# Kernel optimization log

Measured on AMD Instinct MI355X. Metric: run time of the kernel, lower is better.

## Reference

```python
import jax, jax.numpy as jnp
import numpy as np

IMG_H, IMG_W = 800.0, 1280.0
STRIDE = 16
SCALE = 1.0 / STRIDE
P, S = 14, 1              # pooler resolution, sampling ratio
NUM_CLASSES = 80
BBOX_W = (10.0, 10.0, 5.0, 5.0)
SCORE_TH, NMS_TH, MAX_DET, IOU_TH = 0.05, 0.5, 100, 0.5
SCALE_CLAMP = float(np.log(1000.0 / 16.0))


def _make_boxes(key, n_img, n_box):
    k1, k2, k3, k4 = jax.random.split(key, 4)
    x1 = jax.random.uniform(k1, (n_img, n_box)) * (IMG_W - 64.0)
    y1 = jax.random.uniform(k2, (n_img, n_box)) * (IMG_H - 64.0)
    w = jax.random.uniform(k3, (n_img, n_box)) * 300.0 + 16.0
    h = jax.random.uniform(k4, (n_img, n_box)) * 300.0 + 16.0
    x2 = jnp.minimum(x1 + w, IMG_W)
    y2 = jnp.minimum(y1 + h, IMG_H)
    return jnp.stack([x1, y1, x2, y2], axis=-1)


def setup_inputs() -> dict:
    key = jax.random.key(0)
    ks = jax.random.split(key, 6)
    features = jax.random.normal(ks[0], (2, 50, 80, 1024), dtype=jnp.float32)
    proposals = _make_boxes(ks[1], 2, 256)
    gt_boxes = _make_boxes(ks[2], 2, 64)
    gt_classes = jax.random.randint(ks[3], (2, 64), 0, NUM_CLASSES)
    W_cls = jax.random.normal(ks[4], (1024, NUM_CLASSES + 1), dtype=jnp.float32) * 0.01
    b_cls = jnp.zeros((NUM_CLASSES + 1,), jnp.float32)
    W_box = jax.random.normal(ks[5], (1024, 4), dtype=jnp.float32) * 0.01
    b_box = jnp.zeros((4,), jnp.float32)
    return {"features": features, "proposals": proposals, "gt_boxes": gt_boxes,
            "gt_classes": gt_classes, "W_cls": W_cls, "b_cls": b_cls,
            "W_box": W_box, "b_box": b_box}


def pairwise_iou(a, b):
    # a: [G,4], b: [R,4], boxes as (x1,y1,x2,y2) -> [G,R]
    area_a = (a[:, 2] - a[:, 0]) * (a[:, 3] - a[:, 1])
    area_b = (b[:, 2] - b[:, 0]) * (b[:, 3] - b[:, 1])
    lt = jnp.maximum(a[:, None, :2], b[None, :, :2])
    rb = jnp.minimum(a[:, None, 2:], b[None, :, 2:])
    wh = jnp.clip(rb - lt, 0.0)
    inter = wh[..., 0] * wh[..., 1]
    return inter / jnp.maximum(area_a[:, None] + area_b[None, :] - inter, 1e-9)


def roi_align_one(feat, boxes):
    # feat: [H,W,C], boxes: [R,4] in image coords -> pooled [R,P,P,C]
    H, W, C = feat.shape
    b = boxes * SCALE
    x1, y1, x2, y2 = b[:, 0], b[:, 1], b[:, 2], b[:, 3]
    off = (jnp.arange(S, dtype=feat.dtype) + 0.5) / S       # [S]
    grid = jnp.arange(P, dtype=feat.dtype)                   # [P]
    bh = ((y2 - y1) / P)[:, None, None]
    bw = ((x2 - x1) / P)[:, None, None]
    # aligned RoIAlign sample coords (half-pixel offset)
    gy = y1[:, None, None] + (grid[None, :, None] + off[None, None, :]) * bh - 0.5  # [R,P,S]
    gx = x1[:, None, None] + (grid[None, :, None] + off[None, None, :]) * bw - 0.5
    gy = jnp.clip(gy, 0.0, H - 1.0)
    gx = jnp.clip(gx, 0.0, W - 1.0)
    y0 = jnp.floor(gy); x0 = jnp.floor(gx)
    y0i = y0.astype(jnp.int32); x0i = x0.astype(jnp.int32)
    y1i = jnp.minimum(y0i + 1, H - 1); x1i = jnp.minimum(x0i + 1, W - 1)
    ly = gy - y0; lx = gx - x0

    def g(yi, xi):  # cross-product gather -> [R,P,S,P,S,C]
        return feat[yi[:, :, :, None, None], xi[:, None, None, :, :]]

    wy0 = (1.0 - ly)[:, :, :, None, None, None]; wy1 = ly[:, :, :, None, None, None]
    wx0 = (1.0 - lx)[:, None, None, :, :, None]; wx1 = lx[:, None, None, :, :, None]
    val = wy0 * (wx0 * g(y0i, x0i) + wx1 * g(y0i, x1i)) \
        + wy1 * (wx0 * g(y1i, x0i) + wx1 * g(y1i, x1i))
    return val.mean(axis=(2, 4))  # average sampling points per bin -> [R,P,P,C]


def decode_boxes(deltas, boxes):
    wx, wy, ww, wh = BBOX_W
    widths = boxes[..., 2] - boxes[..., 0]
    heights = boxes[..., 3] - boxes[..., 1]
    ctr_x = boxes[..., 0] + 0.5 * widths
    ctr_y = boxes[..., 1] + 0.5 * heights
    dx = deltas[..., 0] / wx
    dy = deltas[..., 1] / wy
    dw = jnp.minimum(deltas[..., 2] / ww, SCALE_CLAMP)
    dh = jnp.minimum(deltas[..., 3] / wh, SCALE_CLAMP)
    pcx = dx * widths + ctr_x
    pcy = dy * heights + ctr_y
    pw = jnp.exp(dw) * widths
    ph = jnp.exp(dh) * heights
    out = jnp.stack([pcx - 0.5 * pw, pcy - 0.5 * ph, pcx + 0.5 * pw, pcy + 0.5 * ph], axis=-1)
    lim = jnp.array([IMG_W, IMG_H, IMG_W, IMG_H], out.dtype)
    return jnp.clip(out, 0.0, lim)


def nms_keep(boxes, scores):
    # greedy class-agnostic NMS, fixed-size keep mask [R]
    R = scores.shape[0]
    order = jnp.argsort(-scores)
    sb = boxes[order]
    iou = pairwise_iou(sb, sb)
    idx = jnp.arange(R)

    def body(i, keep):
        suppressed = jnp.any((idx < i) & keep & (iou[:, i] > NMS_TH))
        return keep.at[i].set(jnp.logical_not(suppressed))

    keep_sorted = jax.lax.fori_loop(0, R, body, jnp.ones((R,), bool))
    return jnp.zeros((R,), bool).at[order].set(keep_sorted)


def reference(features, proposals, gt_boxes, gt_classes, W_cls, b_cls, W_box, b_box):
    N, R = proposals.shape[:2]
    # --- proposal <-> gt matching (training-side labeling) ---
    iou_m = jax.vmap(pairwise_iou)(gt_boxes, proposals)          # [N,G,R]
    matched_vals = iou_m.max(axis=1)
    matched_idxs = iou_m.argmax(axis=1)                          # [N,R]
    match_labels = (matched_vals >= IOU_TH).astype(jnp.int32)    # [N,R] fg=1/bg=0
    # --- RoIAlign pooling on the single C4 feature map ---
    pooled = jax.vmap(roi_align_one)(features, proposals)        # [N,R,P,P,C]
    feat_vec = pooled.mean(axis=(2, 3))                          # res5 surrogate global avg -> [N,R,C]
    # --- box predictor ---
    scores_all = jax.nn.softmax(feat_vec @ W_cls + b_cls, axis=-1)
    fg_scores = scores_all[..., :NUM_CLASSES].max(axis=-1)       # drop background column
    deltas = feat_vec @ W_box + b_box
    boxes = decode_boxes(deltas, proposals)                      # [N,R,4]
    # --- score threshold + NMS + top-k ---
    keep = jax.vmap(nms_keep)(boxes, fg_scores) & (fg_scores > SCORE_TH)
    masked = jnp.where(keep, fg_scores, -jnp.inf)
    rank = jnp.argsort(jnp.argsort(-masked, axis=-1), axis=-1)
    keep = keep & (rank < MAX_DET)
    det = jnp.concatenate([boxes, fg_scores[..., None], keep.astype(boxes.dtype)[..., None]], axis=-1)
    return det, matched_idxs, match_labels
```

## Files before the change

kernel.cpp:

```cpp
#include <hip/hip_runtime.h>
#include <math.h>

#define N_IMG 2
#define R_PROP 256
#define G_GT 64
#define C_CH 1024
#define FH 50
#define FW 80
#define P_POOL 14
#define NCLS 80
#define IMG_W_F 1280.0f
#define IMG_H_F 800.0f
#define SCALE_F 0.0625f
#define SCORE_TH_F 0.05f
#define NMS_TH_F 0.5f
#define IOU_TH_F 0.5f
#define MAX_DET_I 100
#define SCALE_CLAMP_F 4.135166556742356f

__global__ __launch_bounds__(256) void match_kernel(
    const float* __restrict__ proposals,
    const float* __restrict__ gt_boxes,
    float* __restrict__ out_idx,
    float* __restrict__ out_lbl) {
  int t = blockIdx.x * blockDim.x + threadIdx.x;
  if (t >= N_IMG * R_PROP) return;
  int n = t / R_PROP;
  const float* pb = proposals + (size_t)t * 4;
  float bx1 = pb[0], by1 = pb[1], bx2 = pb[2], by2 = pb[3];
  float area_b = (bx2 - bx1) * (by2 - by1);
  float best = -1.0f;
  int bidx = 0;
  const float* gt = gt_boxes + (size_t)n * G_GT * 4;
#pragma unroll 4
  for (int g = 0; g < G_GT; ++g) {
    float gx1 = gt[g * 4 + 0], gy1 = gt[g * 4 + 1];
    float gx2 = gt[g * 4 + 2], gy2 = gt[g * 4 + 3];
    float area_a = (gx2 - gx1) * (gy2 - gy1);
    float ix1 = fmaxf(gx1, bx1), iy1 = fmaxf(gy1, by1);
    float ix2 = fminf(gx2, bx2), iy2 = fminf(gy2, by2);
    float iw = fmaxf(ix2 - ix1, 0.0f), ih = fmaxf(iy2 - iy1, 0.0f);
    float inter = iw * ih;
    float iou = inter / fmaxf(area_a + area_b - inter, 1e-9f);
    if (iou > best) { best = iou; bidx = g; }
  }
  out_idx[t] = (float)bidx;
  out_lbl[t] = (best >= IOU_TH_F) ? 1.0f : 0.0f;
}

__global__ __launch_bounds__(1024) void roi_kernel(
    const float* __restrict__ features,
    const float* __restrict__ proposals,
    float* __restrict__ feat_vec) {
  const int blk = blockIdx.x;
  const int n = blk >> 8;
  const float* feat = features + (size_t)n * (FH * FW * C_CH);
  const int t = threadIdx.x;
  const int c4 = t & 255;
  const int g = t >> 8;

  __shared__ float s_Wy[FH];
  __shared__ float s_Wx[FW];
  __shared__ int s_b[4];
  __shared__ float4 s_red[3][256];

  if (t < FH) s_Wy[t] = 0.0f;
  if (t >= 128 && t < 128 + FW) s_Wx[t - 128] = 0.0f;
  __syncthreads();

  if (t < 2 * P_POOL) {
    const float* pb = proposals + (size_t)blk * 4;
    bool isY = t < P_POOL;
    int i = isY ? t : t - P_POOL;
    float lo = isY ? pb[1] : pb[0];
    float hi = isY ? pb[3] : pb[2];
    float limit = isY ? (float)(FH - 1) : (float)(FW - 1);
    float b1 = lo * SCALE_F, b2 = hi * SCALE_F;
    float bs = (b2 - b1) * (1.0f / P_POOL);
    float gg = b1 + ((float)i + 0.5f) * bs - 0.5f;
    gg = fminf(fmaxf(gg, 0.0f), limit);
    float fl = floorf(gg);
    int i0 = (int)fl;
    int i1 = min(i0 + 1, (int)limit);
    float l = gg - fl;
    if (isY) {
      atomicAdd(&s_Wy[i0], 1.0f - l);
      atomicAdd(&s_Wy[i1], l);
      if (i == 0) s_b[0] = i0;
      if (i == P_POOL - 1) s_b[1] = i1;
    } else {
      atomicAdd(&s_Wx[i0], 1.0f - l);
      atomicAdd(&s_Wx[i1], l);
      if (i == 0) s_b[2] = i0;
      if (i == P_POOL - 1) s_b[3] = i1;
    }
  }
  __syncthreads();

  const int ylo = s_b[0], yhi = s_b[1], xlo = s_b[2], xhi = s_b[3];
  float4 acc = make_float4(0.f, 0.f, 0.f, 0.f);
  for (int y = ylo + g; y <= yhi; y += 4) {
    float wy = s_Wy[y];
    const float4* row = (const float4*)(feat + (size_t)y * (FW * C_CH)) + c4;
#pragma unroll 4
    for (int x = xlo; x <= xhi; ++x) {
      float w = wy * s_Wx[x];
      float4 f = row[x * (C_CH / 4)];
      acc.x += w * f.x;
      acc.y += w * f.y;
      acc.z += w * f.z;
      acc.w += w * f.w;
    }
  }
  if (g > 0) s_red[g - 1][c4] = acc;
  __syncthreads();

  if (g == 0) {
    float4 a0 = s_red[0][c4];
    float4 a1 = s_red[1][c4];
    float4 a2 = s_red[2][c4];
    const float inv = 1.0f / (float)(P_POOL * P_POOL);
    float4 r;
    r.x = (acc.x + a0.x + a1.x + a2.x) * inv;
    r.y = (acc.y + a0.y + a1.y + a2.y) * inv;
    r.z = (acc.z + a0.z + a1.z + a2.z) * inv;
    r.w = (acc.w + a0.w + a1.w + a2.w) * inv;
    ((float4*)(feat_vec + (size_t)blk * C_CH))[c4] = r;
  }
}

__global__ __launch_bounds__(512) void heads_kernel(
    const float* __restrict__ feat_vec,
    const float* __restrict__ proposals,
    const float* __restrict__ W_cls,
    const float* __restrict__ b_cls,
    const float* __restrict__ W_box,
    const float* __restrict__ b_box,
    float* __restrict__ boxes_dec,
    float* __restrict__ scores) {
  const int blk = blockIdx.x;
  const int u = threadIdx.x;
  __shared__ float sf[C_CH];
  __shared__ float s_part[6][85];
  __shared__ float sl[85];
  __shared__ float s_red[8];

  ((float2*)sf)[u] = ((const float2*)(feat_vec + (size_t)blk * C_CH))[u];
  __syncthreads();

  const int kq = u / 85;
  const int j = u - kq * 85;
  if (kq < 6) {
    float acc = 0.0f;
    if (j < 81) {
      const float* __restrict__ w = W_cls + j;
#pragma unroll 8
      for (int k = kq; k < C_CH; k += 6) acc += sf[k] * w[k * 81];
    } else {
      const float* __restrict__ w = W_box + (j - 81);
#pragma unroll 8
      for (int k = kq; k < C_CH; k += 6) acc += sf[k] * w[k * 4];
    }
    s_part[kq][j] = acc;
  }
  __syncthreads();

  if (u < 85) {
    float acc = (u < 81) ? b_cls[u] : b_box[u - 81];
#pragma unroll
    for (int p = 0; p < 6; ++p) acc += s_part[p][u];
    sl[u] = acc;
  }
  __syncthreads();

  if (u < 128) {
    float xm = (u < 81) ? sl[u] : -INFINITY;
    float xf = (u < NCLS) ? sl[u] : -INFINITY;
#pragma unroll
    for (int off = 32; off; off >>= 1) {
      xm = fmaxf(xm, __shfl_down(xm, off, 64));
      xf = fmaxf(xf, __shfl_down(xf, off, 64));
    }
    if ((u & 63) == 0) { s_red[u >> 6] = xm; s_red[2 + (u >> 6)] = xf; }
  }
  __syncthreads();
  const float m = fmaxf(s_red[0], s_red[1]);
  if (u < 128) {
    float xs = (u < 81) ? expf(sl[u] - m) : 0.0f;
#pragma unroll
    for (int off = 32; off; off >>= 1) xs += __shfl_down(xs, off, 64);
    if ((u & 63) == 0) s_red[4 + (u >> 6)] = xs;
  }
  __syncthreads();

  if (u == 0) {
    float sum = s_red[4] + s_red[5];
    float fgm = fmaxf(s_red[2], s_red[3]);
    scores[blk] = expf(fgm - m) / sum;

    const float* pb = proposals + (size_t)blk * 4;
    float w = pb[2] - pb[0], h = pb[3] - pb[1];
    float cx = pb[0] + 0.5f * w, cy = pb[1] + 0.5f * h;
    float dx = sl[81] * 0.1f;
    float dy = sl[82] * 0.1f;
    float dw = fminf(sl[83] * 0.2f, SCALE_CLAMP_F);
    float dh = fminf(sl[84] * 0.2f, SCALE_CLAMP_F);
    float pcx = dx * w + cx, pcy = dy * h + cy;
    float pw = expf(dw) * w, ph = expf(dh) * h;
    float ox1 = fminf(fmaxf(pcx - 0.5f * pw, 0.0f), IMG_W_F);
    float oy1 = fminf(fmaxf(pcy - 0.5f * ph, 0.0f), IMG_H_F);
    float ox2 = fminf(fmaxf(pcx + 0.5f * pw, 0.0f), IMG_W_F);
    float oy2 = fminf(fmaxf(pcy + 0.5f * ph, 0.0f), IMG_H_F);
    float* bd = boxes_dec + (size_t)blk * 4;
    bd[0] = ox1; bd[1] = oy1; bd[2] = ox2; bd[3] = oy2;
  }
}

__global__ __launch_bounds__(1024) void nms_kernel(
    const float* __restrict__ boxes_dec,
    const float* __restrict__ scores,
    float* __restrict__ det) {
  const int n = blockIdx.x;
  const int u = threadIdx.x;
  const int i = u & 255;
  const int q = u >> 8;
  const int j40 = q * 16;

  __shared__ __align__(16) float ss[R_PROP];
  __shared__ float4 sbs[R_PROP];
  __shared__ int s_part[4 * R_PROP];
  __shared__ int s_rank[R_PROP];
  __shared__ __align__(16) unsigned long long s_mask[R_PROP * 4];
  __shared__ unsigned long long s_keep[4];
  __shared__ __align__(16) float sm[R_PROP];

  float4 myb;
  float mys;
  if (q == 0) {
    myb = ((const float4*)boxes_dec)[n * R_PROP + i];
    mys = scores[n * R_PROP + i];
    ss[i] = mys;
  }
  __syncthreads();

  {
    float s = ss[i];
    int cnt = 0;
#pragma unroll
    for (int j4 = j40; j4 < j40 + 16; ++j4) {
      float4 v = ((const float4*)ss)[j4];
      int jb = j4 * 4;
      cnt += (v.x > s) || (v.x == s && jb + 0 < i);
      cnt += (v.y > s) || (v.y == s && jb + 1 < i);
      cnt += (v.z > s) || (v.z == s && jb + 2 < i);
      cnt += (v.w > s) || (v.w == s && jb + 3 < i);
    }
    s_part[q * R_PROP + i] = cnt;
  }
  __syncthreads();
  if (q == 0) {
    int rk = s_part[i] + s_part[R_PROP + i] + s_part[2 * R_PROP + i] +
             s_part[3 * R_PROP + i];
    s_rank[i] = rk;
    sbs[rk] = myb;
  }
  __syncthreads();

  {
    float4 bi = sbs[i];
    float area_i = (bi.z - bi.x) * (bi.w - bi.y);
    unsigned long long m = 0;
    const int j0 = q * 64;
#pragma unroll 8
    for (int jj = 0; jj < 64; ++jj) {
      float4 bj = sbs[j0 + jj];
      float area_j = (bj.z - bj.x) * (bj.w - bj.y);
      float ix1 = fmaxf(bi.x, bj.x), iy1 = fmaxf(bi.y, bj.y);
      float ix2 = fminf(bi.z, bj.z), iy2 = fminf(bi.w, bj.w);
      float iw = fmaxf(ix2 - ix1, 0.0f), ih = fmaxf(iy2 - iy1, 0.0f);
      float inter = iw * ih;
      float iou = inter / fmaxf(area_i + area_j - inter, 1e-9f);
      m |= (iou > NMS_TH_F) ? (1ull << jj) : 0ull;
    }
    s_mask[i * 4 + q] = m;
  }
  __syncthreads();

  if (u == 0) {
    unsigned long long K0 = ~0ull, K1 = ~0ull, K2 = ~0ull, K3 = ~0ull;
#pragma unroll 16
    for (int b = 1; b < 64; ++b) {
      unsigned long long m0 = s_mask[(size_t)b * 4 + 0];
      unsigned long long sup = m0 & K0 & ((1ull << b) - 1ull);
      K0 = sup ? (K0 & ~(1ull << b)) : K0;
    }
#pragma unroll 16
    for (int b = 0; b < 64; ++b) {
      const unsigned long long* mi = &s_mask[(size_t)(64 + b) * 4];
      unsigned long long m0 = mi[0], m1 = mi[1];
      unsigned long long sup = (m0 & K0) | (m1 & K1 & ((1ull << b) - 1ull));
      K1 = sup ? (K1 & ~(1ull << b)) : K1;
    }
#pragma unroll 16
    for (int b = 0; b < 64; ++b) {
      const unsigned long long* mi = &s_mask[(size_t)(128 + b) * 4];
      unsigned long long m0 = mi[0], m1 = mi[1], m2 = mi[2];
      unsigned long long sup =
          (m0 & K0) | (m1 & K1) | (m2 & K2 & ((1ull << b) - 1ull));
      K2 = sup ? (K2 & ~(1ull << b)) : K2;
    }
#pragma unroll 16
    for (int b = 0; b < 64; ++b) {
      const unsigned long long* mi = &s_mask[(size_t)(192 + b) * 4];
      unsigned long long m0 = mi[0], m1 = mi[1], m2 = mi[2], m3 = mi[3];
      unsigned long long sup = (m0 & K0) | (m1 & K1) | (m2 & K2) |
                               (m3 & K3 & ((1ull << b) - 1ull));
      K3 = sup ? (K3 & ~(1ull << b)) : K3;
    }
    s_keep[0] = K0; s_keep[1] = K1; s_keep[2] = K2; s_keep[3] = K3;
  }
  __syncthreads();

  bool kept = false;
  if (q == 0) {
    int rk = s_rank[i];
    kept = ((s_keep[rk >> 6] >> (rk & 63)) & 1ull) && (mys > SCORE_TH_F);
    sm[i] = kept ? mys : -INFINITY;
  }
  __syncthreads();

  {
    float mym = sm[i];
    int cnt = 0;
#pragma unroll
    for (int j4 = j40; j4 < j40 + 16; ++j4) {
      float4 v = ((const float4*)sm)[j4];
      int jb = j4 * 4;
      cnt += (v.x > mym) || (v.x == mym && jb + 0 < i);
      cnt += (v.y > mym) || (v.y == mym && jb + 1 < i);
      cnt += (v.z > mym) || (v.z == mym && jb + 2 < i);
      cnt += (v.w > mym) || (v.w == mym && jb + 3 < i);
    }
    s_part[q * R_PROP + i] = cnt;
  }
  __syncthreads();

  if (q == 0) {
    int rk2 = s_part[i] + s_part[R_PROP + i] + s_part[2 * R_PROP + i] +
              s_part[3 * R_PROP + i];
    kept = kept && (rk2 < MAX_DET_I);
    float* dr = det + ((size_t)n * R_PROP + i) * 6;
    dr[0] = myb.x; dr[1] = myb.y; dr[2] = myb.z; dr[3] = myb.w;
    dr[4] = mys;
    dr[5] = kept ? 1.0f : 0.0f;
  }
}

extern "C" void kernel_launch(void* const* d_in, const int* in_sizes, int n_in,
                              void* d_out, int out_size, void* d_ws, size_t ws_size,
                              hipStream_t stream) {
  const float* features  = (const float*)d_in[0];
  const float* proposals = (const float*)d_in[1];
  const float* gt_boxes  = (const float*)d_in[2];
  const float* W_cls = (const float*)d_in[4];
  const float* b_cls = (const float*)d_in[5];
  const float* W_box = (const float*)d_in[6];
  const float* b_box = (const float*)d_in[7];

  float* out = (float*)d_out;
  float* out_det = out;
  float* out_idx = out + N_IMG * R_PROP * 6;
  float* out_lbl = out_idx + N_IMG * R_PROP;

  float* feat_vec  = (float*)d_ws;
  float* boxes_dec = feat_vec + (size_t)N_IMG * R_PROP * C_CH;
  float* scores    = boxes_dec + (size_t)N_IMG * R_PROP * 4;

  match_kernel<<<2, 256, 0, stream>>>(proposals, gt_boxes, out_idx, out_lbl);
  roi_kernel<<<N_IMG * R_PROP, 1024, 0, stream>>>(features, proposals, feat_vec);
  heads_kernel<<<N_IMG * R_PROP, 512, 0, stream>>>(feat_vec, proposals, W_cls, b_cls,
                                                   W_box, b_box, boxes_dec, scores);
  nms_kernel<<<N_IMG, 1024, 0, stream>>>(boxes_dec, scores, out_det);
}
```

Baseline: 181.9 us.

## Sort RoIs by y-center and map spatial bands to XCDs for L2 locality

Adds a small rank-sort kernel that orders proposals within each image by vertical center. The RoI kernel then remaps block IDs so each of the 8 XCDs gets one image and one vertical band of sorted proposals, aiming to reuse feature rows in each XCD's private L2 instead of refetching from HBM. The change also raises the x-loop unroll and doubles the heads kernel's K-split to 12 partitions with 1024 threads. Costs are an extra kernel launch and a dependence on round-robin block-to-XCD dispatch, which is not guaranteed.

```diff
diff --git a/kernel.cpp b/kernel.cpp
--- a/kernel.cpp
+++ b/kernel.cpp
@@ -17,6 +17,26 @@
 #define IOU_TH_F 0.5f
 #define MAX_DET_I 100
 #define SCALE_CLAMP_F 4.135166556742356f
+
+__global__ __launch_bounds__(512) void sort_kernel(
+    const float* __restrict__ proposals,
+    int* __restrict__ perm) {
+  const int t = threadIdx.x;
+  const int n = t >> 8;
+  __shared__ float cy[N_IMG * R_PROP];
+  const float* pb = proposals + (size_t)t * 4;
+  cy[t] = pb[1] + pb[3];
+  __syncthreads();
+  float my = cy[t];
+  int rk = 0;
+  const int base = n * R_PROP;
+#pragma unroll 8
+  for (int j = base; j < base + R_PROP; ++j) {
+    float cj = cy[j];
+    rk += (cj < my) || (cj == my && j < t);
+  }
+  perm[base + rk] = t & 255;
+}
 
 __global__ __launch_bounds__(256) void match_kernel(
     const float* __restrict__ proposals,
@@ -51,9 +71,15 @@
 __global__ __launch_bounds__(1024) void roi_kernel(
     const float* __restrict__ features,
     const float* __restrict__ proposals,
+    const int* __restrict__ perm,
     float* __restrict__ feat_vec) {
-  const int blk = blockIdx.x;
-  const int n = blk >> 8;
+  const int b = blockIdx.x;
+  const int xcd = b & 7;
+  const int slot = b >> 3;
+  const int n = xcd >> 2;
+  const int band = xcd & 3;
+  const int blk = n * R_PROP + perm[n * R_PROP + band * 64 + slot];
+
   const float* feat = features + (size_t)n * (FH * FW * C_CH);
   const int t = threadIdx.x;
   const int c4 = t & 255;
@@ -102,7 +128,7 @@
   for (int y = ylo + g; y <= yhi; y += 4) {
     float wy = s_Wy[y];
     const float4* row = (const float4*)(feat + (size_t)y * (FW * C_CH)) + c4;
-#pragma unroll 4
+#pragma unroll 8
     for (int x = xlo; x <= xhi; ++x) {
       float w = wy * s_Wx[x];
       float4 f = row[x * (C_CH / 4)];
@@ -129,7 +155,7 @@
   }
 }
 
-__global__ __launch_bounds__(512) void heads_kernel(
+__global__ __launch_bounds__(1024) void heads_kernel(
     const float* __restrict__ feat_vec,
     const float* __restrict__ proposals,
     const float* __restrict__ W_cls,
@@ -141,25 +167,25 @@
   const int blk = blockIdx.x;
   const int u = threadIdx.x;
   __shared__ float sf[C_CH];
-  __shared__ float s_part[6][85];
+  __shared__ float s_part[12][85];
   __shared__ float sl[85];
   __shared__ float s_red[8];
 
-  ((float2*)sf)[u] = ((const float2*)(feat_vec + (size_t)blk * C_CH))[u];
+  sf[u] = feat_vec[(size_t)blk * C_CH + u];
   __syncthreads();
 
   const int kq = u / 85;
   const int j = u - kq * 85;
-  if (kq < 6) {
+  if (kq < 12) {
     float acc = 0.0f;
     if (j < 81) {
       const float* __restrict__ w = W_cls + j;
 #pragma unroll 8
-      for (int k = kq; k < C_CH; k += 6) acc += sf[k] * w[k * 81];
+      for (int k = kq; k < C_CH; k += 12) acc += sf[k] * w[k * 81];
     } else {
       const float* __restrict__ w = W_box + (j - 81);
 #pragma unroll 8
-      for (int k = kq; k < C_CH; k += 6) acc += sf[k] * w[k * 4];
+      for (int k = kq; k < C_CH; k += 12) acc += sf[k] * w[k * 4];
     }
     s_part[kq][j] = acc;
   }
@@ -168,7 +194,7 @@
   if (u < 85) {
     float acc = (u < 81) ? b_cls[u] : b_box[u - 81];
 #pragma unroll
-    for (int p = 0; p < 6; ++p) acc += s_part[p][u];
+    for (int p = 0; p < 12; ++p) acc += s_part[p][u];
     sl[u] = acc;
   }
   __syncthreads();
@@ -375,10 +401,14 @@
   float* feat_vec  = (float*)d_ws;
   float* boxes_dec = feat_vec + (size_t)N_IMG * R_PROP * C_CH;
   float* scores    = boxes_dec + (size_t)N_IMG * R_PROP * 4;
-
+  int*   perm      = (int*)(scores + N_IMG * R_PROP);
+
+  sort_kernel<<<1, 512, 0, stream>>>(proposals, perm);
   match_kernel<<<2, 256, 0, stream>>>(proposals, gt_boxes, out_idx, out_lbl);
-  roi_kernel<<<N_IMG * R_PROP, 1024, 0, stream>>>(features, proposals, feat_vec);
-  heads_kernel<<<N_IMG * R_PROP, 512, 0, stream>>>(feat_vec, proposals, W_cls, b_cls,
-                                                   W_box, b_box, boxes_dec, scores);
+  roi_kernel<<<N_IMG * R_PROP, 1024, 0, stream>>>(features, proposals, perm,
+                                                  feat_vec);
+  heads_kernel<<<N_IMG * R_PROP, 1024, 0, stream>>>(feat_vec, proposals, W_cls,
+                                                    b_cls, W_box, b_box,
+                                                    boxes_dec, scores);
   nms_kernel<<<N_IMG, 1024, 0, stream>>>(boxes_dec, scores, out_det);
 }
```

Result: faster. 171.5 us (-5.7%).
